# Optimization experiments

Measured on AMD Instinct MI355X. Metric: run time of the kernel, lower is better.

Reference implementation:

```python
import jax, jax.numpy as jnp
import numpy as np

N = 50000      # nodes
D = 64         # hidden
EMB = 16       # emb_dims
E = 800000     # edges = N * knn(16)
R2 = 0.3 ** 2  # r^2 at epoch 0
GW = 1.0       # grav_weight at epoch 0
EPS = 1e-5


def _lin_params(k, fi, fo):
    kw, kb = jax.random.split(k)
    W = jax.random.normal(kw, (fi, fo), jnp.float32) / np.sqrt(fi).astype(np.float32)
    b = jax.random.normal(kb, (fo,), jnp.float32) * 0.01
    return W, b


def setup_inputs() -> dict:
    key = jax.random.key(0)
    ks = jax.random.split(key, 16)
    inp = {}
    inp['hidden_features'] = jax.random.normal(ks[0], (N, D), jnp.float32)
    inp['edge_index'] = jax.random.randint(ks[1], (2, E), 0, N, jnp.int32)
    inp['current_epoch'] = 0
    # spatial network: (D+1)->D->D->EMB, each Linear + LayerNorm + ReLU
    for i, (fi, fo) in enumerate([(D + 1, D), (D, D), (D, EMB)]):
        W, b = _lin_params(ks[2 + i], fi, fo)
        inp[f'sW{i}'] = W
        inp[f'sb{i}'] = b
        inp[f'sg{i}'] = jnp.ones((fo,), jnp.float32)
        inp[f'sB{i}'] = jnp.zeros((fo,), jnp.float32)
    # feature network: 2*(D+1)->D->D, each Linear + LayerNorm + ReLU
    for i, (fi, fo) in enumerate([(2 * (D + 1), D), (D, D)]):
        W, b = _lin_params(ks[8 + i], fi, fo)
        inp[f'fW{i}'] = W
        inp[f'fb{i}'] = b
        inp[f'fg{i}'] = jnp.ones((fo,), jnp.float32)
        inp[f'fB{i}'] = jnp.zeros((fo,), jnp.float32)
    return inp


def _ln(x, g, b):
    m = jnp.mean(x, axis=-1, keepdims=True)
    v = jnp.mean((x - m) ** 2, axis=-1, keepdims=True)
    return (x - m) * jax.lax.rsqrt(v + EPS) * g + b


def _blk(x, W, b, g, B):
    return jax.nn.relu(_ln(x @ W + b, g, B))


def reference(hidden_features, edge_index, current_epoch,
              sW0, sb0, sg0, sB0, sW1, sb1, sg1, sB1, sW2, sb2, sg2, sB2,
              fW0, fb0, fg0, fB0, fW1, fb1, fg1, fB1):
    # append per-node mean channel: [N, D] -> [N, D+1]
    h = jnp.concatenate([hidden_features,
                         jnp.mean(hidden_features, axis=1, keepdims=True)], axis=-1)
    # spatial embedding [N, EMB]
    s = _blk(_blk(_blk(h, sW0, sb0, sg0, sB0), sW1, sb1, sg1, sB1), sW2, sb2, sg2, sB2)
    start = edge_index[0]
    end = edge_index[1]
    # gravitational edge weight: exp(-grav_weight * ||s_i - s_j||^2 / r^2)
    d = jnp.sum((s[start] - s[end]) ** 2, axis=-1)  # [E]
    w = jnp.exp(-GW * d / R2)                        # [E]
    # gather -> weight -> scatter_add aggregation
    agg = jax.ops.segment_sum(h[start] * w[:, None], end, num_segments=h.shape[0])
    cat = jnp.concatenate([agg, h], axis=-1)  # [N, 2*(D+1)]
    out = _blk(_blk(cat, fW0, fb0, fg0, fB0), fW1, fb1, fg1, fB1)  # [N, D]
    return out, s
```

## Files before the change

### kernel.cpp

```cpp
#include <hip/hip_runtime.h>
#include <hip/hip_bf16.h>
#include <hip/hip_fp16.h>

#define NN 50000
#define DD 64
#define EMBD 16
#define EE 800000
#define TILES ((NN + 63) / 64)

#define BINW 128
#define NBIN 391
#define CHE 2048
#define NCH 392
#define CAPA 32
#define LCAP 64

#define OW_S0 0
#define OW_S1 6656
#define OW_S2 11264
#define OW_F0 12416
#define OW_F1 23168
#define NWB   27776

typedef short s16x8 __attribute__((ext_vector_type(8)));
typedef float f32x4 __attribute__((ext_vector_type(4)));
typedef _Float16 h16x8 __attribute__((ext_vector_type(8)));

__device__ __forceinline__ unsigned short f2b(float x) {
  unsigned u = __float_as_uint(x);
  return (unsigned short)((u + 0x7FFFu + ((u >> 16) & 1u)) >> 16);
}

__device__ __forceinline__ float b2f(unsigned short u) {
  return __uint_as_float(((unsigned)u) << 16);
}

__device__ __forceinline__ unsigned short f2h(float x) {
  return __half_as_ushort(__float2half(x));
}

__device__ __forceinline__ float h2f(unsigned short u) {
  return (float)__ushort_as_half(u);
}

__device__ __forceinline__ float wred64f(float v) {
  v += __shfl_xor(v, 1);  v += __shfl_xor(v, 2);  v += __shfl_xor(v, 4);
  v += __shfl_xor(v, 8);  v += __shfl_xor(v, 16); v += __shfl_xor(v, 32);
  return v;
}

__global__ __launch_bounds__(256)
void GravConv3556_prep_k(const float* __restrict__ sW0, const float* __restrict__ sW1,
                         const float* __restrict__ sW2, const float* __restrict__ fW0,
                         const float* __restrict__ fW1, unsigned short* __restrict__ wb)
{
  int i0 = blockIdx.x * 256 + threadIdx.x;
  int st = gridDim.x * 256;
  for (int i = i0; i < 64 * 104; i += st) {
    int n = i / 104, k = i % 104;
    wb[OW_S0 + i] = (k < 65) ? f2b(sW0[k * 64 + n]) : (unsigned short)0;
  }
  for (int i = i0; i < 64 * 72; i += st) {
    int n = i / 72, k = i % 72;
    wb[OW_S1 + i] = (k < 64) ? f2b(sW1[k * 64 + n]) : (unsigned short)0;
  }
  for (int i = i0; i < 16 * 72; i += st) {
    int n = i / 72, k = i % 72;
    wb[OW_S2 + i] = (k < 64) ? f2b(sW2[k * 16 + n]) : (unsigned short)0;
  }
  for (int i = i0; i < 64 * 168; i += st) {
    int n = i / 168, k = i % 168;
    wb[OW_F0 + i] = (k < 130) ? f2b(fW0[k * 64 + n]) : (unsigned short)0;
  }
  for (int i = i0; i < 64 * 72; i += st) {
    int n = i / 72, k = i % 72;
    wb[OW_F1 + i] = (k < 64) ? f2b(fW1[k * 64 + n]) : (unsigned short)0;
  }
}

__global__ __launch_bounds__(256)
void GravConv3556_binpart_k(const int* __restrict__ ei,
                            unsigned* __restrict__ seg,
                            unsigned char* __restrict__ cnts)
{
  __shared__ int bc[NBIN];
  int tid = threadIdx.x;
  int chunk = blockIdx.x;
  for (int i = tid; i < NBIN; i += 256) bc[i] = 0;
  __syncthreads();
  int e0 = chunk * CHE;
  int e1 = e0 + CHE; if (e1 > EE) e1 = EE;
  unsigned* segc = seg + (size_t)chunk * NBIN * CAPA;
  for (int e = e0 + tid; e < e1; e += 256) {
    int a = ei[e];
    int b = ei[EE + e];
    int bin = b >> 7;
    int pos = atomicAdd(&bc[bin], 1);
    if (pos < CAPA) segc[bin * CAPA + pos] = ((unsigned)a << 7) | (unsigned)(b & 127);
  }
  __syncthreads();
  for (int i = tid; i < NBIN; i += 256) {
    int c = bc[i]; if (c > CAPA) c = CAPA;
    cnts[(size_t)i * NCH + chunk] = (unsigned char)c;
  }
}

#define XROW 104
__global__ __launch_bounds__(256)
void GravConv3556_spatial_k(const float* __restrict__ hidden,
    const unsigned short* __restrict__ wb,
    const float* __restrict__ sb0, const float* __restrict__ sg0, const float* __restrict__ sB0,
    const float* __restrict__ sb1, const float* __restrict__ sg1, const float* __restrict__ sB1,
    const float* __restrict__ sb2, const float* __restrict__ sg2, const float* __restrict__ sB2,
    float* __restrict__ s_out, unsigned short* __restrict__ s16,
    unsigned short* __restrict__ hid16)
{
  __shared__ unsigned short X[64 * XROW];
  __shared__ unsigned short W0[64 * XROW];
  __shared__ unsigned short W1[64 * 72];
  __shared__ unsigned short W2[16 * 72];
  int tid = threadIdx.x;
  int lane = tid & 63;
  int wv = tid >> 6;
  int c = lane & 15;
  int q = lane >> 4;
  int base = blockIdx.x * 64;

  {
    const uint4* g = (const uint4*)(wb + OW_S0); uint4* l = (uint4*)W0;
    for (int i = tid; i < 832; i += 256) l[i] = g[i];
    g = (const uint4*)(wb + OW_S1); l = (uint4*)W1;
    for (int i = tid; i < 576; i += 256) l[i] = g[i];
    g = (const uint4*)(wb + OW_S2); l = (uint4*)W2;
    for (int i = tid; i < 144; i += 256) l[i] = g[i];
  }
  for (int i = 0; i < 16; i++) {
    int m = wv * 16 + i;
    int node = base + m; if (node >= NN) node = NN - 1;
    float x = hidden[(size_t)node * 64 + lane];
    float mean = wred64f(x) * (1.0f / 64.0f);
    X[m * XROW + lane] = f2b(x);
    hid16[(size_t)node * 64 + lane] = f2h(x);
    if (lane == 0) X[m * XROW + 64] = f2b(mean);
    if (lane < 39) X[m * XROW + 65 + lane] = 0;
  }
  __syncthreads();

  int mrow = wv * 16 + c;
  float z[16];

  {
    s16x8 a[3];
    #pragma unroll
    for (int kc = 0; kc < 3; kc++)
      a[kc] = *(const s16x8*)(X + mrow * XROW + kc * 32 + q * 8);
    #pragma unroll
    for (int nt = 0; nt < 4; nt++) {
      f32x4 acc = {0.f, 0.f, 0.f, 0.f};
      #pragma unroll
      for (int kc = 0; kc < 3; kc++) {
        s16x8 b = *(const s16x8*)(W0 + (nt * 16 + c) * XROW + kc * 32 + q * 8);
        acc = __builtin_amdgcn_mfma_f32_16x16x32_bf16(a[kc], b, acc, 0, 0, 0);
      }
      float bias = sb0[nt * 16 + c];
      #pragma unroll
      for (int reg = 0; reg < 4; reg++) z[nt * 4 + reg] = acc[reg] + bias;
    }
    #pragma unroll
    for (int reg = 0; reg < 4; reg++) {
      float s1 = z[reg] + z[4 + reg] + z[8 + reg] + z[12 + reg];
      float s2 = z[reg] * z[reg] + z[4 + reg] * z[4 + reg]
               + z[8 + reg] * z[8 + reg] + z[12 + reg] * z[12 + reg];
      s1 += __shfl_xor(s1, 1); s2 += __shfl_xor(s2, 1);
      s1 += __shfl_xor(s1, 2); s2 += __shfl_xor(s2, 2);
      s1 += __shfl_xor(s1, 4); s2 += __shfl_xor(s2, 4);
      s1 += __shfl_xor(s1, 8); s2 += __shfl_xor(s2, 8);
      float mu = s1 * (1.0f / 64.0f);
      float rs = rsqrtf(fmaxf(s2 * (1.0f / 64.0f) - mu * mu, 0.f) + 1e-5f);
      int m = wv * 16 + q * 4 + reg;
      #pragma unroll
      for (int nt = 0; nt < 4; nt++) {
        int n = nt * 16 + c;
        float y = fmaxf(fmaf((z[nt * 4 + reg] - mu) * rs, sg0[n], sB0[n]), 0.f);
        X[m * XROW + n] = f2b(y);
      }
    }
  }

  {
    s16x8 a[2];
    #pragma unroll
    for (int kc = 0; kc < 2; kc++)
      a[kc] = *(const s16x8*)(X + mrow * XROW + kc * 32 + q * 8);
    #pragma unroll
    for (int nt = 0; nt < 4; nt++) {
      f32x4 acc = {0.f, 0.f, 0.f, 0.f};
      #pragma unroll
      for (int kc = 0; kc < 2; kc++) {
        s16x8 b = *(const s16x8*)(W1 + (nt * 16 + c) * 72 + kc * 32 + q * 8);
        acc = __builtin_amdgcn_mfma_f32_16x16x32_bf16(a[kc], b, acc, 0, 0, 0);
      }
      float bias = sb1[nt * 16 + c];
      #pragma unroll
      for (int reg = 0; reg < 4; reg++) z[nt * 4 + reg] = acc[reg] + bias;
    }
    #pragma unroll
    for (int reg = 0; reg < 4; reg++) {
      float s1 = z[reg] + z[4 + reg] + z[8 + reg] + z[12 + reg];
      float s2 = z[reg] * z[reg] + z[4 + reg] * z[4 + reg]
               + z[8 + reg] * z[8 + reg] + z[12 + reg] * z[12 + reg];
      s1 += __shfl_xor(s1, 1); s2 += __shfl_xor(s2, 1);
      s1 += __shfl_xor(s1, 2); s2 += __shfl_xor(s2, 2);
      s1 += __shfl_xor(s1, 4); s2 += __shfl_xor(s2, 4);
      s1 += __shfl_xor(s1, 8); s2 += __shfl_xor(s2, 8);
      float mu = s1 * (1.0f / 64.0f);
      float rs = rsqrtf(fmaxf(s2 * (1.0f / 64.0f) - mu * mu, 0.f) + 1e-5f);
      int m = wv * 16 + q * 4 + reg;
      #pragma unroll
      for (int nt = 0; nt < 4; nt++) {
        int n = nt * 16 + c;
        float y = fmaxf(fmaf((z[nt * 4 + reg] - mu) * rs, sg1[n], sB1[n]), 0.f);
        X[m * XROW + n] = f2b(y);
      }
    }
  }

  {
    s16x8 a[2];
    #pragma unroll
    for (int kc = 0; kc < 2; kc++)
      a[kc] = *(const s16x8*)(X + mrow * XROW + kc * 32 + q * 8);
    f32x4 acc = {0.f, 0.f, 0.f, 0.f};
    #pragma unroll
    for (int kc = 0; kc < 2; kc++) {
      s16x8 b = *(const s16x8*)(W2 + c * 72 + kc * 32 + q * 8);
      acc = __builtin_amdgcn_mfma_f32_16x16x32_bf16(a[kc], b, acc, 0, 0, 0);
    }
    float bias = sb2[c];
    float z4[4];
    #pragma unroll
    for (int reg = 0; reg < 4; reg++) z4[reg] = acc[reg] + bias;
    #pragma unroll
    for (int reg = 0; reg < 4; reg++) {
      float s1 = z4[reg], s2 = z4[reg] * z4[reg];
      s1 += __shfl_xor(s1, 1); s2 += __shfl_xor(s2, 1);
      s1 += __shfl_xor(s1, 2); s2 += __shfl_xor(s2, 2);
      s1 += __shfl_xor(s1, 4); s2 += __shfl_xor(s2, 4);
      s1 += __shfl_xor(s1, 8); s2 += __shfl_xor(s2, 8);
      float mu = s1 * (1.0f / 16.0f);
      float rs = rsqrtf(fmaxf(s2 * (1.0f / 16.0f) - mu * mu, 0.f) + 1e-5f);
      float y = fmaxf(fmaf((z4[reg] - mu) * rs, sg2[c], sB2[c]), 0.f);
      int node = base + wv * 16 + q * 4 + reg;
      if (node < NN) {
        s_out[(size_t)node * 16 + c] = y;
        s16[(size_t)node * 16 + c] = f2h(y);
      }
    }
  }
}

__global__ __launch_bounds__(1024)
void GravConv3556_agg_k(const unsigned short* __restrict__ hid16,
                        const unsigned short* __restrict__ s16,
                        const unsigned* __restrict__ seg,
                        const unsigned char* __restrict__ cnts,
                        unsigned short* __restrict__ aggr)
{
  __shared__ unsigned short lbuk[BINW * LCAP];
  __shared__ int lcnt[BINW];
  int tid = threadIdx.x;
  int lane = tid & 63;
  int wv = tid >> 6;
  int bin = blockIdx.x;
  int n0 = bin << 7;
  int nb = NN - n0; if (nb > BINW) nb = BINW;
  for (int i = tid; i < BINW; i += 1024) lcnt[i] = 0;
  __syncthreads();

  const unsigned char* cr = cnts + (size_t)bin * NCH;
  for (int c = wv; c < NCH; c += 16) {
    int k = cr[c];
    if (lane < k) {
      unsigned e = seg[((size_t)c * NBIN + bin) * CAPA + lane];
      int dl = (int)(e & 127u);
      int pos = atomicAdd(&lcnt[dl], 1);
      if (pos < LCAP) lbuk[dl * LCAP + pos] = (unsigned short)(e >> 7);
    }
  }
  __syncthreads();

  const _Float16* hid = (const _Float16*)hid16;
  const _Float16* s = (const _Float16*)s16;
  for (int rn = wv; rn < nb; rn += 16) {
    int n = n0 + rn;
    int m = lcnt[rn]; if (m > LCAP) m = LCAP;
    unsigned pr = 0;
    if (lane < m) {
      int a = lbuk[rn * LCAP + lane];
      const h16x8* sa = (const h16x8*)(s + (size_t)a * 16);
      const h16x8* sn = (const h16x8*)(s + (size_t)n * 16);
      h16x8 p0 = sa[0], p1 = sa[1];
      h16x8 q0 = sn[0], q1 = sn[1];
      float d = 0.f;
      #pragma unroll
      for (int t = 0; t < 8; t++) {
        float u = (float)p0[t] - (float)q0[t];
        d = fmaf(u, u, d);
        float v = (float)p1[t] - (float)q1[t];
        d = fmaf(v, v, d);
      }
      float w = __expf(d * (-1.0f / 0.09f));
      pr = ((unsigned)a << 16) | (unsigned)f2h(w);
    }
    float xa0 = 0.f, xa1 = 0.f, xa2 = 0.f, xa3 = 0.f;
#define GSTEP(q, ACC) { int jj = jb + (q); int jc = jj < m ? jj : m - 1;        \
    unsigned u_ = (unsigned)__builtin_amdgcn_readlane((int)pr, jc);             \
    int   a_ = (int)(u_ >> 16);                                                 \
    float w_ = (jj < m) ? h2f((unsigned short)(u_ & 0xFFFFu)) : 0.0f;           \
    ACC = fmaf(w_, (float)hid[(size_t)a_ * 64 + lane], ACC); }
    for (int jb = 0; jb < m; jb += 8) {
      GSTEP(0, xa0) GSTEP(1, xa1) GSTEP(2, xa2) GSTEP(3, xa3)
      GSTEP(4, xa0) GSTEP(5, xa1) GSTEP(6, xa2) GSTEP(7, xa3)
    }
#undef GSTEP
    aggr[(size_t)n * 64 + lane] = f2b((xa0 + xa1) + (xa2 + xa3));
  }
}

#define CROW 168
__global__ __launch_bounds__(256)
void GravConv3556_feature_k(const float* __restrict__ hidden,
    const unsigned short* __restrict__ aggr, const unsigned short* __restrict__ wb,
    const float* __restrict__ fb0, const float* __restrict__ fg0, const float* __restrict__ fB0,
    const float* __restrict__ fb1, const float* __restrict__ fg1, const float* __restrict__ fB1,
    float* __restrict__ out)
{
  __shared__ unsigned short catB[64 * CROW];
  __shared__ unsigned short W0T[64 * CROW];
  __shared__ unsigned short W1T[64 * 72];
  int tid = threadIdx.x;
  int lane = tid & 63;
  int wv = tid >> 6;
  int c = lane & 15;
  int q = lane >> 4;
  int base = blockIdx.x * 64;

  {
    const uint4* g = (const uint4*)(wb + OW_F0); uint4* l = (uint4*)W0T;
    for (int i = tid; i < 1344; i += 256) l[i] = g[i];
    g = (const uint4*)(wb + OW_F1); l = (uint4*)W1T;
    for (int i = tid; i < 576; i += 256) l[i] = g[i];
  }

  for (int i = 0; i < 16; i++) {
    int m = wv * 16 + i;
    int node = base + m; if (node >= NN) node = NN - 1;
    unsigned short ra = aggr[(size_t)node * 64 + lane];
    float xa = b2f(ra);
    float mA = wred64f(xa) * (1.0f / 64.0f);
    catB[m * CROW + lane] = ra;
    float xh = hidden[(size_t)node * 64 + lane];
    float mB = wred64f(xh) * (1.0f / 64.0f);
    catB[m * CROW + 65 + lane] = f2b(xh);
    if (lane == 0) {
      catB[m * CROW + 64] = f2b(mA);
      catB[m * CROW + 129] = f2b(mB);
    }
    if (lane < 38) catB[m * CROW + 130 + lane] = 0;
  }
  __syncthreads();

  int mrow = wv * 16 + c;

  s16x8 a0[5];
  #pragma unroll
  for (int kc = 0; kc < 5; kc++)
    a0[kc] = *(const s16x8*)(catB + mrow * CROW + kc * 32 + q * 8);

  float z[16];
  #pragma unroll
  for (int nt = 0; nt < 4; nt++) {
    f32x4 acc = {0.f, 0.f, 0.f, 0.f};
    #pragma unroll
    for (int kc = 0; kc < 5; kc++) {
      s16x8 b = *(const s16x8*)(W0T + (nt * 16 + c) * CROW + kc * 32 + q * 8);
      acc = __builtin_amdgcn_mfma_f32_16x16x32_bf16(a0[kc], b, acc, 0, 0, 0);
    }
    float bias = fb0[nt * 16 + c];
    #pragma unroll
    for (int reg = 0; reg < 4; reg++) z[nt * 4 + reg] = acc[reg] + bias;
  }
  #pragma unroll
  for (int reg = 0; reg < 4; reg++) {
    float s1 = z[reg] + z[4 + reg] + z[8 + reg] + z[12 + reg];
    float s2 = z[reg] * z[reg] + z[4 + reg] * z[4 + reg]
             + z[8 + reg] * z[8 + reg] + z[12 + reg] * z[12 + reg];
    s1 += __shfl_xor(s1, 1); s2 += __shfl_xor(s2, 1);
    s1 += __shfl_xor(s1, 2); s2 += __shfl_xor(s2, 2);
    s1 += __shfl_xor(s1, 4); s2 += __shfl_xor(s2, 4);
    s1 += __shfl_xor(s1, 8); s2 += __shfl_xor(s2, 8);
    float mu = s1 * (1.0f / 64.0f);
    float rs = rsqrtf(fmaxf(s2 * (1.0f / 64.0f) - mu * mu, 0.f) + 1e-5f);
    int m = wv * 16 + q * 4 + reg;
    #pragma unroll
    for (int nt = 0; nt < 4; nt++) {
      int n = nt * 16 + c;
      float y = fmaxf(fmaf((z[nt * 4 + reg] - mu) * rs, fg0[n], fB0[n]), 0.f);
      catB[m * CROW + n] = f2b(y);
    }
  }

  s16x8 a1[2];
  #pragma unroll
  for (int kc = 0; kc < 2; kc++)
    a1[kc] = *(const s16x8*)(catB + mrow * CROW + kc * 32 + q * 8);

  #pragma unroll
  for (int nt = 0; nt < 4; nt++) {
    f32x4 acc = {0.f, 0.f, 0.f, 0.f};
    #pragma unroll
    for (int kc = 0; kc < 2; kc++) {
      s16x8 b = *(const s16x8*)(W1T + (nt * 16 + c) * 72 + kc * 32 + q * 8);
      acc = __builtin_amdgcn_mfma_f32_16x16x32_bf16(a1[kc], b, acc, 0, 0, 0);
    }
    float bias = fb1[nt * 16 + c];
    #pragma unroll
    for (int reg = 0; reg < 4; reg++) z[nt * 4 + reg] = acc[reg] + bias;
  }
  #pragma unroll
  for (int reg = 0; reg < 4; reg++) {
    float s1 = z[reg] + z[4 + reg] + z[8 + reg] + z[12 + reg];
    float s2 = z[reg] * z[reg] + z[4 + reg] * z[4 + reg]
             + z[8 + reg] * z[8 + reg] + z[12 + reg] * z[12 + reg];
    s1 += __shfl_xor(s1, 1); s2 += __shfl_xor(s2, 1);
    s1 += __shfl_xor(s1, 2); s2 += __shfl_xor(s2, 2);
    s1 += __shfl_xor(s1, 4); s2 += __shfl_xor(s2, 4);
    s1 += __shfl_xor(s1, 8); s2 += __shfl_xor(s2, 8);
    float mu = s1 * (1.0f / 64.0f);
    float rs = rsqrtf(fmaxf(s2 * (1.0f / 64.0f) - mu * mu, 0.f) + 1e-5f);
    int node = base + wv * 16 + q * 4 + reg;
    if (node < NN) {
      #pragma unroll
      for (int nt = 0; nt < 4; nt++) {
        int n = nt * 16 + c;
        float y = fmaxf(fmaf((z[nt * 4 + reg] - mu) * rs, fg1[n], fB1[n]), 0.f);
        out[(size_t)node * 64 + n] = y;
      }
    }
  }
}

extern "C" void kernel_launch(void* const* d_in, const int* in_sizes, int n_in,
                              void* d_out, int out_size, void* d_ws, size_t ws_size,
                              hipStream_t stream) {
  const float* hidden = (const float*)d_in[0];
  const int*   ei     = (const int*)d_in[1];
  const float *sW0 = (const float*)d_in[3],  *sb0 = (const float*)d_in[4],
              *sg0 = (const float*)d_in[5],  *sB0 = (const float*)d_in[6];
  const float *sW1 = (const float*)d_in[7],  *sb1 = (const float*)d_in[8],
              *sg1 = (const float*)d_in[9],  *sB1 = (const float*)d_in[10];
  const float *sW2 = (const float*)d_in[11], *sb2 = (const float*)d_in[12],
              *sg2 = (const float*)d_in[13], *sB2 = (const float*)d_in[14];
  const float *fW0 = (const float*)d_in[15], *fb0 = (const float*)d_in[16],
              *fg0 = (const float*)d_in[17], *fB0 = (const float*)d_in[18];
  const float *fW1 = (const float*)d_in[19], *fb1 = (const float*)d_in[20],
              *fg1 = (const float*)d_in[21], *fB1 = (const float*)d_in[22];

  float* out   = (float*)d_out;
  float* s_out = out + (size_t)NN * 64;

  unsigned* seg = (unsigned*)d_ws;
  unsigned char* cnts = (unsigned char*)(seg + (size_t)NCH * NBIN * CAPA);
  unsigned short* aggr = (unsigned short*)
      (((uintptr_t)(cnts + (size_t)NBIN * NCH) + 15) & ~(uintptr_t)15);
  unsigned short* hid16 = aggr + (size_t)NN * 64;
  unsigned short* s16   = hid16 + (size_t)NN * 64;
  unsigned short* wbuf  = s16 + (size_t)NN * 16;

  GravConv3556_prep_k<<<64, 256, 0, stream>>>(sW0, sW1, sW2, fW0, fW1, wbuf);
  GravConv3556_binpart_k<<<NCH, 256, 0, stream>>>(ei, seg, cnts);
  GravConv3556_spatial_k<<<TILES, 256, 0, stream>>>(hidden, wbuf,
      sb0, sg0, sB0, sb1, sg1, sB1, sb2, sg2, sB2, s_out, s16, hid16);
  GravConv3556_agg_k<<<NBIN, 1024, 0, stream>>>(hid16, s16, seg, cnts, aggr);
  GravConv3556_feature_k<<<TILES, 256, 0, stream>>>(hidden, aggr, wbuf,
      fb0, fg0, fB0, fb1, fg1, fB1, out);
}
```

Before: 224.7 us.

## Fuse aggregation with feature MLP and merge weight prep into binning kernel

Merges the weight-conversion kernel and the edge binning kernel into one launch, using extra blocks for the prep work. Halves the destination bin width to 64 nodes so that one 1024-thread aggregation block covers exactly one 64-node feature tile. The aggregated rows then go straight into shared memory for the two-layer feature MLP, which removes the bf16 aggr round-trip through global memory and one kernel launch. The trade-offs: only 4 of the 16 waves do the MFMA stage, the per-block LDS footprint is larger, and with 196 chunks of 4096 edges each per-(chunk, bin) count is larger, so truncation at CAPA is more likely.

```diff
diff --git a/kernel.cpp b/kernel.cpp
--- a/kernel.cpp
+++ b/kernel.cpp
@@ -8,12 +8,13 @@
 #define EE 800000
 #define TILES ((NN + 63) / 64)
 
-#define BINW 128
-#define NBIN 391
-#define CHE 2048
-#define NCH 392
+#define BINW 64
+#define NBIN 782
+#define CHE 4096
+#define NCH 196
 #define CAPA 32
 #define LCAP 64
+#define PREPB 64
 
 #define OW_S0 0
 #define OW_S1 6656
@@ -49,57 +50,57 @@
   return v;
 }
 
-__global__ __launch_bounds__(256)
-void GravConv3556_prep_k(const float* __restrict__ sW0, const float* __restrict__ sW1,
-                         const float* __restrict__ sW2, const float* __restrict__ fW0,
-                         const float* __restrict__ fW1, unsigned short* __restrict__ wb)
+__global__ __launch_bounds__(512)
+void GravConv3556_prebin_k(const int* __restrict__ ei,
+                           const float* __restrict__ sW0, const float* __restrict__ sW1,
+                           const float* __restrict__ sW2, const float* __restrict__ fW0,
+                           const float* __restrict__ fW1,
+                           unsigned short* __restrict__ wb,
+                           unsigned* __restrict__ seg,
+                           unsigned char* __restrict__ cnts)
 {
-  int i0 = blockIdx.x * 256 + threadIdx.x;
-  int st = gridDim.x * 256;
-  for (int i = i0; i < 64 * 104; i += st) {
-    int n = i / 104, k = i % 104;
-    wb[OW_S0 + i] = (k < 65) ? f2b(sW0[k * 64 + n]) : (unsigned short)0;
-  }
-  for (int i = i0; i < 64 * 72; i += st) {
-    int n = i / 72, k = i % 72;
-    wb[OW_S1 + i] = (k < 64) ? f2b(sW1[k * 64 + n]) : (unsigned short)0;
-  }
-  for (int i = i0; i < 16 * 72; i += st) {
-    int n = i / 72, k = i % 72;
-    wb[OW_S2 + i] = (k < 64) ? f2b(sW2[k * 16 + n]) : (unsigned short)0;
-  }
-  for (int i = i0; i < 64 * 168; i += st) {
-    int n = i / 168, k = i % 168;
-    wb[OW_F0 + i] = (k < 130) ? f2b(fW0[k * 64 + n]) : (unsigned short)0;
-  }
-  for (int i = i0; i < 64 * 72; i += st) {
-    int n = i / 72, k = i % 72;
-    wb[OW_F1 + i] = (k < 64) ? f2b(fW1[k * 64 + n]) : (unsigned short)0;
-  }
-}
-
-__global__ __launch_bounds__(256)
-void GravConv3556_binpart_k(const int* __restrict__ ei,
-                            unsigned* __restrict__ seg,
-                            unsigned char* __restrict__ cnts)
-{
+  int tid = threadIdx.x;
+  if ((int)blockIdx.x >= NCH) {
+    int i0 = ((int)blockIdx.x - NCH) * 512 + tid;
+    int st = PREPB * 512;
+    for (int i = i0; i < 64 * 104; i += st) {
+      int n = i / 104, k = i % 104;
+      wb[OW_S0 + i] = (k < 65) ? f2b(sW0[k * 64 + n]) : (unsigned short)0;
+    }
+    for (int i = i0; i < 64 * 72; i += st) {
+      int n = i / 72, k = i % 72;
+      wb[OW_S1 + i] = (k < 64) ? f2b(sW1[k * 64 + n]) : (unsigned short)0;
+    }
+    for (int i = i0; i < 16 * 72; i += st) {
+      int n = i / 72, k = i % 72;
+      wb[OW_S2 + i] = (k < 64) ? f2b(sW2[k * 16 + n]) : (unsigned short)0;
+    }
+    for (int i = i0; i < 64 * 168; i += st) {
+      int n = i / 168, k = i % 168;
+      wb[OW_F0 + i] = (k < 130) ? f2b(fW0[k * 64 + n]) : (unsigned short)0;
+    }
+    for (int i = i0; i < 64 * 72; i += st) {
+      int n = i / 72, k = i % 72;
+      wb[OW_F1 + i] = (k < 64) ? f2b(fW1[k * 64 + n]) : (unsigned short)0;
+    }
+    return;
+  }
   __shared__ int bc[NBIN];
-  int tid = threadIdx.x;
   int chunk = blockIdx.x;
-  for (int i = tid; i < NBIN; i += 256) bc[i] = 0;
+  for (int i = tid; i < NBIN; i += 512) bc[i] = 0;
   __syncthreads();
   int e0 = chunk * CHE;
   int e1 = e0 + CHE; if (e1 > EE) e1 = EE;
   unsigned* segc = seg + (size_t)chunk * NBIN * CAPA;
-  for (int e = e0 + tid; e < e1; e += 256) {
+  for (int e = e0 + tid; e < e1; e += 512) {
     int a = ei[e];
     int b = ei[EE + e];
-    int bin = b >> 7;
+    int bin = b >> 6;
     int pos = atomicAdd(&bc[bin], 1);
-    if (pos < CAPA) segc[bin * CAPA + pos] = ((unsigned)a << 7) | (unsigned)(b & 127);
-  }
-  __syncthreads();
-  for (int i = tid; i < NBIN; i += 256) {
+    if (pos < CAPA) segc[bin * CAPA + pos] = ((unsigned)a << 6) | (unsigned)(b & 63);
+  }
+  __syncthreads();
+  for (int i = tid; i < NBIN; i += 512) {
     int c = bc[i]; if (c > CAPA) c = CAPA;
     cnts[(size_t)i * NCH + chunk] = (unsigned char)c;
   }
@@ -259,22 +260,34 @@
   }
 }
 
+#define CROW 168
 __global__ __launch_bounds__(1024)
-void GravConv3556_agg_k(const unsigned short* __restrict__ hid16,
-                        const unsigned short* __restrict__ s16,
-                        const unsigned* __restrict__ seg,
-                        const unsigned char* __restrict__ cnts,
-                        unsigned short* __restrict__ aggr)
+void GravConv3556_featagg_k(const float* __restrict__ hidden,
+    const unsigned short* __restrict__ hid16, const unsigned short* __restrict__ s16,
+    const unsigned* __restrict__ seg, const unsigned char* __restrict__ cnts,
+    const unsigned short* __restrict__ wb,
+    const float* __restrict__ fb0, const float* __restrict__ fg0, const float* __restrict__ fB0,
+    const float* __restrict__ fb1, const float* __restrict__ fg1, const float* __restrict__ fB1,
+    float* __restrict__ out)
 {
-  __shared__ unsigned short lbuk[BINW * LCAP];
-  __shared__ int lcnt[BINW];
+  __shared__ unsigned short catB[64 * CROW];
+  __shared__ unsigned short W0T[64 * CROW];
+  __shared__ unsigned short W1T[64 * 72];
+  __shared__ unsigned short lbuk[64 * LCAP];
+  __shared__ int lcnt[64];
   int tid = threadIdx.x;
   int lane = tid & 63;
   int wv = tid >> 6;
   int bin = blockIdx.x;
-  int n0 = bin << 7;
-  int nb = NN - n0; if (nb > BINW) nb = BINW;
-  for (int i = tid; i < BINW; i += 1024) lcnt[i] = 0;
+  int base = bin * 64;
+
+  {
+    const uint4* g = (const uint4*)(wb + OW_F0); uint4* l = (uint4*)W0T;
+    for (int i = tid; i < 1344; i += 1024) l[i] = g[i];
+    g = (const uint4*)(wb + OW_F1); l = (uint4*)W1T;
+    for (int i = tid; i < 576; i += 1024) l[i] = g[i];
+  }
+  for (int i = tid; i < 64; i += 1024) lcnt[i] = 0;
   __syncthreads();
 
   const unsigned char* cr = cnts + (size_t)bin * NCH;
@@ -282,23 +295,24 @@
     int k = cr[c];
     if (lane < k) {
       unsigned e = seg[((size_t)c * NBIN + bin) * CAPA + lane];
-      int dl = (int)(e & 127u);
+      int dl = (int)(e & 63u);
       int pos = atomicAdd(&lcnt[dl], 1);
-      if (pos < LCAP) lbuk[dl * LCAP + pos] = (unsigned short)(e >> 7);
+      if (pos < LCAP) lbuk[dl * LCAP + pos] = (unsigned short)(e >> 6);
     }
   }
   __syncthreads();
 
   const _Float16* hid = (const _Float16*)hid16;
   const _Float16* s = (const _Float16*)s16;
-  for (int rn = wv; rn < nb; rn += 16) {
-    int n = n0 + rn;
+  for (int rn = wv; rn < 64; rn += 16) {
+    int node = base + rn;
+    int nclamp = node < NN ? node : NN - 1;
     int m = lcnt[rn]; if (m > LCAP) m = LCAP;
     unsigned pr = 0;
     if (lane < m) {
       int a = lbuk[rn * LCAP + lane];
       const h16x8* sa = (const h16x8*)(s + (size_t)a * 16);
-      const h16x8* sn = (const h16x8*)(s + (size_t)n * 16);
+      const h16x8* sn = (const h16x8*)(s + (size_t)node * 16);
       h16x8 p0 = sa[0], p1 = sa[1];
       h16x8 q0 = sn[0], q1 = sn[1];
       float d = 0.f;
@@ -323,128 +337,99 @@
       GSTEP(4, xa0) GSTEP(5, xa1) GSTEP(6, xa2) GSTEP(7, xa3)
     }
 #undef GSTEP
-    aggr[(size_t)n * 64 + lane] = f2b((xa0 + xa1) + (xa2 + xa3));
-  }
-}
-
-#define CROW 168
-__global__ __launch_bounds__(256)
-void GravConv3556_feature_k(const float* __restrict__ hidden,
-    const unsigned short* __restrict__ aggr, const unsigned short* __restrict__ wb,
-    const float* __restrict__ fb0, const float* __restrict__ fg0, const float* __restrict__ fB0,
-    const float* __restrict__ fb1, const float* __restrict__ fg1, const float* __restrict__ fB1,
-    float* __restrict__ out)
-{
-  __shared__ unsigned short catB[64 * CROW];
-  __shared__ unsigned short W0T[64 * CROW];
-  __shared__ unsigned short W1T[64 * 72];
-  int tid = threadIdx.x;
-  int lane = tid & 63;
-  int wv = tid >> 6;
-  int c = lane & 15;
-  int q = lane >> 4;
-  int base = blockIdx.x * 64;
-
-  {
-    const uint4* g = (const uint4*)(wb + OW_F0); uint4* l = (uint4*)W0T;
-    for (int i = tid; i < 1344; i += 256) l[i] = g[i];
-    g = (const uint4*)(wb + OW_F1); l = (uint4*)W1T;
-    for (int i = tid; i < 576; i += 256) l[i] = g[i];
-  }
-
-  for (int i = 0; i < 16; i++) {
-    int m = wv * 16 + i;
-    int node = base + m; if (node >= NN) node = NN - 1;
-    unsigned short ra = aggr[(size_t)node * 64 + lane];
-    float xa = b2f(ra);
+    float xa = (xa0 + xa1) + (xa2 + xa3);
     float mA = wred64f(xa) * (1.0f / 64.0f);
-    catB[m * CROW + lane] = ra;
-    float xh = hidden[(size_t)node * 64 + lane];
+    catB[rn * CROW + lane] = f2b(xa);
+    float xh = hidden[(size_t)nclamp * 64 + lane];
     float mB = wred64f(xh) * (1.0f / 64.0f);
-    catB[m * CROW + 65 + lane] = f2b(xh);
+    catB[rn * CROW + 65 + lane] = f2b(xh);
     if (lane == 0) {
-      catB[m * CROW + 64] = f2b(mA);
-      catB[m * CROW + 129] = f2b(mB);
-    }
-    if (lane < 38) catB[m * CROW + 130 + lane] = 0;
-  }
-  __syncthreads();
-
-  int mrow = wv * 16 + c;
-
-  s16x8 a0[5];
-  #pragma unroll
-  for (int kc = 0; kc < 5; kc++)
-    a0[kc] = *(const s16x8*)(catB + mrow * CROW + kc * 32 + q * 8);
-
-  float z[16];
-  #pragma unroll
-  for (int nt = 0; nt < 4; nt++) {
-    f32x4 acc = {0.f, 0.f, 0.f, 0.f};
-    #pragma unroll
-    for (int kc = 0; kc < 5; kc++) {
-      s16x8 b = *(const s16x8*)(W0T + (nt * 16 + c) * CROW + kc * 32 + q * 8);
-      acc = __builtin_amdgcn_mfma_f32_16x16x32_bf16(a0[kc], b, acc, 0, 0, 0);
-    }
-    float bias = fb0[nt * 16 + c];
-    #pragma unroll
-    for (int reg = 0; reg < 4; reg++) z[nt * 4 + reg] = acc[reg] + bias;
-  }
-  #pragma unroll
-  for (int reg = 0; reg < 4; reg++) {
-    float s1 = z[reg] + z[4 + reg] + z[8 + reg] + z[12 + reg];
-    float s2 = z[reg] * z[reg] + z[4 + reg] * z[4 + reg]
-             + z[8 + reg] * z[8 + reg] + z[12 + reg] * z[12 + reg];
-    s1 += __shfl_xor(s1, 1); s2 += __shfl_xor(s2, 1);
-    s1 += __shfl_xor(s1, 2); s2 += __shfl_xor(s2, 2);
-    s1 += __shfl_xor(s1, 4); s2 += __shfl_xor(s2, 4);
-    s1 += __shfl_xor(s1, 8); s2 += __shfl_xor(s2, 8);
-    float mu = s1 * (1.0f / 64.0f);
-    float rs = rsqrtf(fmaxf(s2 * (1.0f / 64.0f) - mu * mu, 0.f) + 1e-5f);
-    int m = wv * 16 + q * 4 + reg;
+      catB[rn * CROW + 64] = f2b(mA);
+      catB[rn * CROW + 129] = f2b(mB);
+    }
+    if (lane < 38) catB[rn * CROW + 130 + lane] = 0;
+  }
+  __syncthreads();
+
+  if (wv < 4) {
+    int c = lane & 15;
+    int q = lane >> 4;
+    int mrow = wv * 16 + c;
+
+    s16x8 a0[5];
+    #pragma unroll
+    for (int kc = 0; kc < 5; kc++)
+      a0[kc] = *(const s16x8*)(catB + mrow * CROW + kc * 32 + q * 8);
+
+    float z[16];
     #pragma unroll
     for (int nt = 0; nt < 4; nt++) {
-      int n = nt * 16 + c;
-      float y = fmaxf(fmaf((z[nt * 4 + reg] - mu) * rs, fg0[n], fB0[n]), 0.f);
-      catB[m * CROW + n] = f2b(y);
-    }
-  }
-
-  s16x8 a1[2];
-  #pragma unroll
-  for (int kc = 0; kc < 2; kc++)
-    a1[kc] = *(const s16x8*)(catB + mrow * CROW + kc * 32 + q * 8);
-
-  #pragma unroll
-  for (int nt = 0; nt < 4; nt++) {
-    f32x4 acc = {0.f, 0.f, 0.f, 0.f};
-    #pragma unroll
-    for (int kc = 0; kc < 2; kc++) {
-      s16x8 b = *(const s16x8*)(W1T + (nt * 16 + c) * 72 + kc * 32 + q * 8);
-      acc = __builtin_amdgcn_mfma_f32_16x16x32_bf16(a1[kc], b, acc, 0, 0, 0);
-    }
-    float bias = fb1[nt * 16 + c];
-    #pragma unroll
-    for (int reg = 0; reg < 4; reg++) z[nt * 4 + reg] = acc[reg] + bias;
-  }
-  #pragma unroll
-  for (int reg = 0; reg < 4; reg++) {
-    float s1 = z[reg] + z[4 + reg] + z[8 + reg] + z[12 + reg];
-    float s2 = z[reg] * z[reg] + z[4 + reg] * z[4 + reg]
-             + z[8 + reg] * z[8 + reg] + z[12 + reg] * z[12 + reg];
-    s1 += __shfl_xor(s1, 1); s2 += __shfl_xor(s2, 1);
-    s1 += __shfl_xor(s1, 2); s2 += __shfl_xor(s2, 2);
-    s1 += __shfl_xor(s1, 4); s2 += __shfl_xor(s2, 4);
-    s1 += __shfl_xor(s1, 8); s2 += __shfl_xor(s2, 8);
-    float mu = s1 * (1.0f / 64.0f);
-    float rs = rsqrtf(fmaxf(s2 * (1.0f / 64.0f) - mu * mu, 0.f) + 1e-5f);
-    int node = base + wv * 16 + q * 4 + reg;
-    if (node < NN) {
+      f32x4 acc = {0.f, 0.f, 0.f, 0.f};
+      #pragma unroll
+      for (int kc = 0; kc < 5; kc++) {
+        s16x8 b = *(const s16x8*)(W0T + (nt * 16 + c) * CROW + kc * 32 + q * 8);
+        acc = __builtin_amdgcn_mfma_f32_16x16x32_bf16(a0[kc], b, acc, 0, 0, 0);
+      }
+      float bias = fb0[nt * 16 + c];
+      #pragma unroll
+      for (int reg = 0; reg < 4; reg++) z[nt * 4 + reg] = acc[reg] + bias;
+    }
+    #pragma unroll
+    for (int reg = 0; reg < 4; reg++) {
+      float s1 = z[reg] + z[4 + reg] + z[8 + reg] + z[12 + reg];
+      float s2 = z[reg] * z[reg] + z[4 + reg] * z[4 + reg]
+               + z[8 + reg] * z[8 + reg] + z[12 + reg] * z[12 + reg];
+      s1 += __shfl_xor(s1, 1); s2 += __shfl_xor(s2, 1);
+      s1 += __shfl_xor(s1, 2); s2 += __shfl_xor(s2, 2);
+      s1 += __shfl_xor(s1, 4); s2 += __shfl_xor(s2, 4);
+      s1 += __shfl_xor(s1, 8); s2 += __shfl_xor(s2, 8);
+      float mu = s1 * (1.0f / 64.0f);
+      float rs = rsqrtf(fmaxf(s2 * (1.0f / 64.0f) - mu * mu, 0.f) + 1e-5f);
+      int m = wv * 16 + q * 4 + reg;
       #pragma unroll
       for (int nt = 0; nt < 4; nt++) {
         int n = nt * 16 + c;
-        float y = fmaxf(fmaf((z[nt * 4 + reg] - mu) * rs, fg1[n], fB1[n]), 0.f);
-        out[(size_t)node * 64 + n] = y;
+        float y = fmaxf(fmaf((z[nt * 4 + reg] - mu) * rs, fg0[n], fB0[n]), 0.f);
+        catB[m * CROW + n] = f2b(y);
+      }
+    }
+
+    s16x8 a1[2];
+    #pragma unroll
+    for (int kc = 0; kc < 2; kc++)
+      a1[kc] = *(const s16x8*)(catB + mrow * CROW + kc * 32 + q * 8);
+
+    #pragma unroll
+    for (int nt = 0; nt < 4; nt++) {
+      f32x4 acc = {0.f, 0.f, 0.f, 0.f};
+      #pragma unroll
+      for (int kc = 0; kc < 2; kc++) {
+        s16x8 b = *(const s16x8*)(W1T + (nt * 16 + c) * 72 + kc * 32 + q * 8);
+        acc = __builtin_amdgcn_mfma_f32_16x16x32_bf16(a1[kc], b, acc, 0, 0, 0);
+      }
+      float bias = fb1[nt * 16 + c];
+      #pragma unroll
+      for (int reg = 0; reg < 4; reg++) z[nt * 4 + reg] = acc[reg] + bias;
+    }
+    #pragma unroll
+    for (int reg = 0; reg < 4; reg++) {
+      float s1 = z[reg] + z[4 + reg] + z[8 + reg] + z[12 + reg];
+      float s2 = z[reg] * z[reg] + z[4 + reg] * z[4 + reg]
+               + z[8 + reg] * z[8 + reg] + z[12 + reg] * z[12 + reg];
+      s1 += __shfl_xor(s1, 1); s2 += __shfl_xor(s2, 1);
+      s1 += __shfl_xor(s1, 2); s2 += __shfl_xor(s2, 2);
+      s1 += __shfl_xor(s1, 4); s2 += __shfl_xor(s2, 4);
+      s1 += __shfl_xor(s1, 8); s2 += __shfl_xor(s2, 8);
+      float mu = s1 * (1.0f / 64.0f);
+      float rs = rsqrtf(fmaxf(s2 * (1.0f / 64.0f) - mu * mu, 0.f) + 1e-5f);
+      int node = base + wv * 16 + q * 4 + reg;
+      if (node < NN) {
+        #pragma unroll
+        for (int nt = 0; nt < 4; nt++) {
+          int n = nt * 16 + c;
+          float y = fmaxf(fmaf((z[nt * 4 + reg] - mu) * rs, fg1[n], fB1[n]), 0.f);
+          out[(size_t)node * 64 + n] = y;
+        }
       }
     }
   }
@@ -471,17 +456,15 @@
 
   unsigned* seg = (unsigned*)d_ws;
   unsigned char* cnts = (unsigned char*)(seg + (size_t)NCH * NBIN * CAPA);
-  unsigned short* aggr = (unsigned short*)
+  unsigned short* hid16 = (unsigned short*)
       (((uintptr_t)(cnts + (size_t)NBIN * NCH) + 15) & ~(uintptr_t)15);
-  unsigned short* hid16 = aggr + (size_t)NN * 64;
   unsigned short* s16   = hid16 + (size_t)NN * 64;
   unsigned short* wbuf  = s16 + (size_t)NN * 16;
 
-  GravConv3556_prep_k<<<64, 256, 0, stream>>>(sW0, sW1, sW2, fW0, fW1, wbuf);
-  GravConv3556_binpart_k<<<NCH, 256, 0, stream>>>(ei, seg, cnts);
+  GravConv3556_prebin_k<<<NCH + PREPB, 512, 0, stream>>>(ei, sW0, sW1, sW2, fW0, fW1,
+                                                         wbuf, seg, cnts);
   GravConv3556_spatial_k<<<TILES, 256, 0, stream>>>(hidden, wbuf,
       sb0, sg0, sB0, sb1, sg1, sB1, sb2, sg2, sB2, s_out, s16, hid16);
-  GravConv3556_agg_k<<<NBIN, 1024, 0, stream>>>(hid16, s16, seg, cnts, aggr);
-  GravConv3556_feature_k<<<TILES, 256, 0, stream>>>(hidden, aggr, wbuf,
-      fb0, fg0, fB0, fb1, fg1, fB1, out);
-}
+  GravConv3556_featagg_k<<<NBIN, 1024, 0, stream>>>(hidden, hid16, s16, seg, cnts,
+      wbuf, fb0, fg0, fB0, fb1, fg1, fB1, out);
+}
```

Result: faster. 199.3 us (-11.3%).
